# Kernel optimization log

Hardware: AMD Instinct MI355X
Metric: run time of the kernel (lower is better)

## Reference

```python
import jax, jax.numpy as jnp
import numpy as np

B, C, H, W = 4, 3, 256, 256
NSH = 33          # number of shearlets for scales=3 (pyshearlab default)
THETA = 1.0       # init kwarg theta


def setup_inputs() -> dict:
    key = jax.random.key(0)
    k1, k2, k3, k4, k5 = jax.random.split(key, 5)
    target = jax.random.normal(k1, (B, C, H, W), dtype=jnp.float32)
    prediction = jax.random.normal(k2, (B, C, H, W), dtype=jnp.float32)
    interval_radius = jax.random.uniform(k3, (B, C, H, W), dtype=jnp.float32)
    # real Fourier-domain shearlet filter bank (stand-in for pyshearlab system)
    filters = jax.random.normal(k4, (NSH, H, W), dtype=jnp.float32)
    # per-filter RMS normalizers, bounded away from zero
    rms = jax.random.uniform(k5, (NSH,), dtype=jnp.float32) + 0.5
    return {"target": target, "prediction": prediction,
            "interval_radius": interval_radius, "filters": filters, "rms": rms}


def _shearlet_coeffs(x, filters, rms):
    # x: [B,C,H,W]; filters: [NSH,H,W] real spectral filters.
    # SLsheardec2D: coeffs_j = ifft2(fft2(x) * conj(psi_j)); psi real -> conj no-op.
    xf = jnp.fft.fft2(x)                                        # [B,C,H,W] complex
    coeffs = jnp.fft.ifft2(xf[:, :, None] * filters[None, None]).real  # [B,C,NSH,H,W]
    coeffs = coeffs[:, :, :-1] / rms[:-1][None, None, :, None, None]   # drop last filter
    # original flattens [H,W,nsh-1] in (H,W,j) order
    coeffs = jnp.transpose(coeffs, (0, 1, 3, 4, 2))             # [B,C,H,W,NSH-1]
    return coeffs.reshape(x.shape[0], x.shape[1], -1)           # [B,C,H*W*(NSH-1)]


def reference(target, prediction, interval_radius, filters, rms):
    tc = _shearlet_coeffs(target, filters, rms)
    pc = _shearlet_coeffs(prediction, filters, rms)
    radius = _shearlet_coeffs(interval_radius, filters, rms)
    residual = jnp.abs(tc - pc)
    R = THETA - jax.nn.relu(THETA - jax.nn.relu(residual - radius))
    Rm = jnp.mean(R, axis=(1, 2))                               # [B]
    Rd = jnp.std(R, axis=(1, 2), ddof=1)                        # torch.std is unbiased
    return (R, Rm, Rd)
```

## Files before the change

### kernel.cpp

```cpp
#include <hip/hip_runtime.h>
#include <hip/hip_fp16.h>
#include <math.h>

#define HW 256
#define BCN 12
#define NF 32
#define R_TOTAL 25165824

__device__ __forceinline__ float2 h2f(unsigned u){
  return __half22float2(__builtin_bit_cast(__half2, u));
}
__device__ __forceinline__ unsigned f2h(float2 v){
  return __builtin_bit_cast(unsigned, __floats2half2_rn(v.x, v.y));
}

__device__ __forceinline__ float4 c4add(float4 a,float4 b){
  return make_float4(a.x+b.x,a.y+b.y,a.z+b.z,a.w+b.w);}
__device__ __forceinline__ float4 c4sub(float4 a,float4 b){
  return make_float4(a.x-b.x,a.y-b.y,a.z-b.z,a.w-b.w);}
__device__ __forceinline__ float4 c4mul(float2 w, float4 v){
  return make_float4(w.x*v.x - w.y*v.y, w.x*v.y + w.y*v.x,
                     w.x*v.z - w.y*v.w, w.x*v.w + w.y*v.z);}
__device__ __forceinline__ float4 fma4s(float s, float4 t, float4 o){
  return make_float4(fmaf(s,t.x,o.x), fmaf(s,t.y,o.y),
                     fmaf(s,t.z,o.z), fmaf(s,t.w,o.w));}
template<int SGN>
__device__ __forceinline__ float4 rots(float4 v){
  return (SGN>0) ? make_float4(-v.y,v.x,-v.w,v.z)
                 : make_float4(v.y,-v.x,v.w,-v.z);}
__device__ __forceinline__ float4 shfl_xor4(float4 v,int m){
  return make_float4(__shfl_xor(v.x,m,64),__shfl_xor(v.y,m,64),
                     __shfl_xor(v.z,m,64),__shfl_xor(v.w,m,64));}

template<int CTRL>
__device__ __forceinline__ float dpp_f(float x){
  return __builtin_bit_cast(float,
    __builtin_amdgcn_update_dpp(0, __builtin_bit_cast(int, x), CTRL, 0xF, 0xF, true));
}
template<int CTRL>
__device__ __forceinline__ float4 dpp4(float4 v){
  return make_float4(dpp_f<CTRL>(v.x), dpp_f<CTRL>(v.y),
                     dpp_f<CTRL>(v.z), dpp_f<CTRL>(v.w));
}
__device__ __forceinline__ float xor4_f(float x){
  return dpp_f<0x141>(dpp_f<0x1B>(x));
}

struct Tw {
  float2 V2,V4,V8,V16,V32,t64,t128;
  float s1,s2,s4,s8,s16,s32;
};
template<int SGN>
__device__ __forceinline__ void make_tw(Tw &T, int lane){
  const float g = (SGN>0)? 1.0f : -1.0f;
  float s,c;
  sincospif((float)(lane&1)*0.5f,&s,&c);
  T.V2  = (lane&2)?  make_float2(c,g*s) : make_float2(1.f,0.f);
  sincospif((float)(lane&3)*0.25f,&s,&c);
  T.V4  = (lane&4)?  make_float2(c,g*s) : make_float2(1.f,0.f);
  sincospif((float)(lane&7)*0.125f,&s,&c);
  T.V8  = (lane&8)?  make_float2(c,g*s) : make_float2(1.f,0.f);
  sincospif((float)(lane&15)*0.0625f,&s,&c);
  T.V16 = (lane&16)? make_float2(c,g*s) : make_float2(1.f,0.f);
  sincospif((float)(lane&31)*0.03125f,&s,&c);
  T.V32 = (lane&32)? make_float2(c,g*s) : make_float2(1.f,0.f);
  sincospif((float)lane*(1.0f/64.0f),&s,&c);  T.t64 = make_float2(c,g*s);
  sincospif((float)lane*(1.0f/128.0f),&s,&c); T.t128= make_float2(c,g*s);
  T.s1=(lane&1)?-1.f:1.f;  T.s2=(lane&2)?-1.f:1.f;  T.s4=(lane&4)?-1.f:1.f;
  T.s8=(lane&8)?-1.f:1.f;  T.s16=(lane&16)?-1.f:1.f; T.s32=(lane&32)?-1.f:1.f;
}

template<int SGN>
__device__ __forceinline__ void fft4(float4 e[4], const Tw &T, int lane){
#pragma unroll
  for(int r=0;r<4;++r){
    float4 o = dpp4<0xB1>(e[r]);
    e[r] = fma4s(T.s1, e[r], o);
  }
#pragma unroll
  for(int r=0;r<4;++r){
    float4 t = c4mul(T.V2, e[r]);
    float4 o = dpp4<0x4E>(t);
    e[r] = fma4s(T.s2, t, o);
  }
#pragma unroll
  for(int r=0;r<4;++r){
    float4 t = c4mul(T.V4, e[r]);
    float4 o = shfl_xor4(t,4);
    e[r] = fma4s(T.s4, t, o);
  }
#pragma unroll
  for(int r=0;r<4;++r){
    float4 t = c4mul(T.V8, e[r]);
    float4 o = dpp4<0x128>(t);
    e[r] = fma4s(T.s8, t, o);
  }
#pragma unroll
  for(int r=0;r<4;++r){
    float4 t = c4mul(T.V16, e[r]);
    float4 o = shfl_xor4(t,16);
    e[r] = fma4s(T.s16, t, o);
  }
#pragma unroll
  for(int r=0;r<4;++r){
    float4 t = c4mul(T.V32, e[r]);
    float4 o = shfl_xor4(t,32);
    e[r] = fma4s(T.s32, t, o);
  }
  float4 t = c4mul(T.t64, e[1]); e[1]=c4sub(e[0],t); e[0]=c4add(e[0],t);
  t = c4mul(T.t64, e[3]); e[3]=c4sub(e[2],t); e[2]=c4add(e[2],t);
  t = c4mul(T.t128, e[2]); e[2]=c4sub(e[0],t); e[0]=c4add(e[0],t);
  t = c4mul(T.t128, e[3]); t = rots<SGN>(t);
  e[3]=c4sub(e[1],t); e[1]=c4add(e[1],t);
}

__global__ __launch_bounds__(256) void k_prep(const float* __restrict__ filt,
                                              const float* __restrict__ rms,
                                              __half* __restrict__ psiP){
  __shared__ float tile[32][257];
  int j = blockIdx.y, u0 = blockIdx.x<<5, tid = threadIdx.x;
  float rinv = 1.0f / rms[j];
  const float* fj = filt + (size_t)j*HW*HW;
#pragma unroll 4
  for(int k=0;k<32;++k){
    int u = u0+k, v = tid;
    int u2 = (HW-u)&255, v2 = (HW-v)&255;
    tile[k][v] = (fj[(size_t)u*HW+v] + fj[(size_t)u2*HW+v2])*0.5f*rinv;
  }
  __syncthreads();
  __half* pj = psiP + (size_t)j*HW*HW + u0;
#pragma unroll 4
  for(int it=0; it<32; ++it){
    int v = (it<<3) + (tid>>5), ul = tid&31;
    pj[(size_t)v*HW + ul] = __float2half(tile[ul][v]);
  }
}

__global__ __launch_bounds__(256) void k_fwd_rows(const float* __restrict__ tg,
                                                  const float* __restrict__ pr,
                                                  const float* __restrict__ ir,
                                                  float2* __restrict__ X1){
  int tid=threadIdx.x, lane=tid&63, wv=tid>>6;
  Tw T; make_tw<-1>(T,lane);
  int bc = blockIdx.x>>5;
  int h0 = ((blockIdx.x&31)<<3) | (wv<<1);
  size_t b0 = ((size_t)bc*HW+h0)*HW;
  size_t b1 = b0 + HW;
  int cb4 = (int)((__brev((unsigned)lane)>>26)<<2);
  float4 t0 = *(const float4*)(tg+b0+cb4);
  float4 p0 = *(const float4*)(pr+b0+cb4);
  float4 i0 = *(const float4*)(ir+b0+cb4);
  float4 t1 = *(const float4*)(tg+b1+cb4);
  float4 p1 = *(const float4*)(pr+b1+cb4);
  float4 i1 = *(const float4*)(ir+b1+cb4);
  float4 e[4];
  e[0]=make_float4(t0.x-p0.x, i0.x, t1.x-p1.x, i1.x);
  e[2]=make_float4(t0.y-p0.y, i0.y, t1.y-p1.y, i1.y);
  e[1]=make_float4(t0.z-p0.z, i0.z, t1.z-p1.z, i1.z);
  e[3]=make_float4(t0.w-p0.w, i0.w, t1.w-p1.w, i1.w);
  fft4<-1>(e,T,lane);
#pragma unroll
  for(int r=0;r<4;++r){
    X1[b0 + (r<<6)+lane] = make_float2(e[r].x,e[r].y);
    X1[b1 + (r<<6)+lane] = make_float2(e[r].z,e[r].w);
  }
}

__global__ __launch_bounds__(256) void k_fwd_cols(const float2* __restrict__ X1,
                                                  unsigned* __restrict__ T2h){
  int tid=threadIdx.x, lane=tid&63, wv=tid>>6;
  Tw T; make_tw<-1>(T,lane);
  int bc = blockIdx.x>>5;
  int v0 = ((blockIdx.x&31)<<3) | (wv<<1);
  int b4 = (int)((__brev((unsigned)lane)>>26)<<2);
  const float2* xb = X1 + (size_t)bc*HW*HW + v0;
  float4 L0 = *(const float4*)(xb + (size_t)(b4+0)*HW);
  float4 L1 = *(const float4*)(xb + (size_t)(b4+1)*HW);
  float4 L2 = *(const float4*)(xb + (size_t)(b4+2)*HW);
  float4 L3 = *(const float4*)(xb + (size_t)(b4+3)*HW);
  float4 e[4];
  e[0]=L0; e[2]=L1; e[1]=L2; e[3]=L3;
  fft4<-1>(e,T,lane);
  const float s = 1.0f/65536.0f;
  unsigned* t0 = T2h + (size_t)bc*HW*HW + (size_t)v0*HW;
#pragma unroll
  for(int r=0;r<4;++r){
    int u = (r<<6)+lane;
    t0[u]    = f2h(make_float2(e[r].x*s, e[r].y*s));
    t0[HW+u] = f2h(make_float2(e[r].z*s, e[r].w*s));
  }
}

__global__ __launch_bounds__(256) void k_b1(const unsigned* __restrict__ T2h,
                                            const __half* __restrict__ psiP,
                                            unsigned* __restrict__ Zh,
                                            int bc0){
  int tid=threadIdx.x, lane=tid&63, wv=tid>>6;
  Tw T; make_tw<1>(T,lane);
  int j  = blockIdx.x;
  int vt = blockIdx.y<<4;
  int bcl= blockIdx.z;
  int bc = bc0 + bcl;
  int cb = __brev((unsigned)lane)>>26;
  int u0 = cb<<2;
  int vb = vt + (wv<<2);
  const unsigned* tb  = T2h  + (size_t)bc*HW*HW + u0;
  const __half*   pjb = psiP + (size_t)j*HW*HW + u0;
  float4 ea[4], eb[4];
#pragma unroll
  for(int p=0;p<2;++p){
    int v0 = vb + (p<<1);
    uint4 tA = *(const uint4*)(tb + (size_t)v0*HW);
    uint4 tB = *(const uint4*)(tb + (size_t)(v0+1)*HW);
    uint2 puA = *(const uint2*)(pjb + (size_t)v0*HW);
    uint2 puB = *(const uint2*)(pjb + (size_t)(v0+1)*HW);
    float2 pA01 = h2f(puA.x), pA23 = h2f(puA.y);
    float2 pB01 = h2f(puB.x), pB23 = h2f(puB.y);
    float2 a0=h2f(tA.x), a1=h2f(tA.y), a2=h2f(tA.z), a3=h2f(tA.w);
    float2 c0=h2f(tB.x), c1=h2f(tB.y), c2=h2f(tB.z), c3=h2f(tB.w);
    float4* e = p? eb : ea;
    e[0]=make_float4(a0.x*pA01.x, a0.y*pA01.x, c0.x*pB01.x, c0.y*pB01.x);
    e[2]=make_float4(a1.x*pA01.y, a1.y*pA01.y, c1.x*pB01.y, c1.y*pB01.y);
    e[1]=make_float4(a2.x*pA23.x, a2.y*pA23.x, c2.x*pB23.x, c2.y*pB23.x);
    e[3]=make_float4(a3.x*pA23.y, a3.y*pA23.y, c3.x*pB23.y, c3.y*pB23.y);
    fft4<1>(e,T,lane);
  }
  unsigned* zb = Zh + ((size_t)bcl*HW*NF + j)*HW + vb;
#pragma unroll
  for(int r=0;r<4;++r){
    int h = (r<<6)+lane;
    *(uint4*)(zb + (size_t)h*NF*HW) =
      make_uint4(f2h(make_float2(ea[r].x,ea[r].y)),
                 f2h(make_float2(ea[r].z,ea[r].w)),
                 f2h(make_float2(eb[r].x,eb[r].y)),
                 f2h(make_float2(eb[r].z,eb[r].w)));
  }
}

__global__ __launch_bounds__(256) void k_b2(const unsigned* __restrict__ Zh,
                                            float* __restrict__ out,
                                            double* __restrict__ part,
                                            int bc0){
  __shared__ float Rt[16*260];
  __shared__ double redS[4], redQ[4];
  int tid=threadIdx.x, lane=tid&63, wv=tid>>6;
  int h = blockIdx.x;
  int bcl = blockIdx.y;
  int bc = bc0 + bcl;
  int cb = __brev((unsigned)lane)>>26;
  const unsigned* zb = Zh + ((size_t)bcl*HW + h)*NF*HW + (cb<<2);
  uint4 L[8];
#pragma unroll
  for(int c=0;c<4;++c){
    int jl0 = (wv<<2) + ((c&1)<<1);
    int j0  = ((c>>1)<<4) + jl0;
    L[2*c]   = *(const uint4*)(zb + (size_t)j0*HW);
    L[2*c+1] = *(const uint4*)(zb + (size_t)(j0+1)*HW);
  }
  Tw T; make_tw<1>(T,lane);
  float lsum=0.0f, lsq=0.0f;
  float* ob = out + (size_t)bc*(HW*HW*NF) + (size_t)h*(HW*NF);
  float R[4][8];
#pragma unroll
  for(int c=0;c<4;++c){
    uint4 z0 = L[2*c];
    uint4 z1 = L[2*c+1];
    float2 a0=h2f(z0.x),a1=h2f(z0.y),a2=h2f(z0.z),a3=h2f(z0.w);
    float2 c0=h2f(z1.x),c1=h2f(z1.y),c2=h2f(z1.z),c3=h2f(z1.w);
    float4 e[4];
    e[0]=make_float4(a0.x,a0.y,c0.x,c0.y);
    e[2]=make_float4(a1.x,a1.y,c1.x,c1.y);
    e[1]=make_float4(a2.x,a2.y,c2.x,c2.y);
    e[3]=make_float4(a3.x,a3.y,c3.x,c3.y);
    fft4<1>(e,T,lane);
#pragma unroll
    for(int r=0;r<4;++r){
      float t1 = fmaxf(fabsf(e[r].x)-e[r].y, 0.0f);
      float R0 = 1.0f - fmaxf(1.0f-t1, 0.0f);
      float t2 = fmaxf(fabsf(e[r].z)-e[r].w, 0.0f);
      float R1 = 1.0f - fmaxf(1.0f-t2, 0.0f);
      R[c][r*2]   = R0;
      R[c][r*2+1] = R1;
      lsum += R0; lsum += R1;
      lsq = fmaf(R0,R0,lsq); lsq = fmaf(R1,R1,lsq);
    }
  }
#pragma unroll
  for(int jh=0;jh<2;++jh){
    if(jh) __syncthreads();
#pragma unroll
    for(int p=0;p<2;++p){
      int c = jh*2+p;
      int jl0 = (wv<<2)+(p<<1);
#pragma unroll
      for(int r=0;r<4;++r){
        int w = (r<<6)+lane;
        Rt[jl0*260 + w]     = R[c][r*2];
        Rt[(jl0+1)*260 + w] = R[c][r*2+1];
      }
    }
    __syncthreads();
    float vals[16];
#pragma unroll
    for(int k=0;k<16;++k) vals[k]=Rt[k*260+tid];
    float4* dst = (float4*)(ob + (size_t)tid*NF + (jh<<4));
    dst[0]=make_float4(vals[0],vals[1],vals[2],vals[3]);
    dst[1]=make_float4(vals[4],vals[5],vals[6],vals[7]);
    dst[2]=make_float4(vals[8],vals[9],vals[10],vals[11]);
    dst[3]=make_float4(vals[12],vals[13],vals[14],vals[15]);
  }
  lsum += __shfl_xor(lsum,32,64);          lsq += __shfl_xor(lsq,32,64);
  lsum += __shfl_xor(lsum,16,64);          lsq += __shfl_xor(lsq,16,64);
  lsum += dpp_f<0x128>(lsum);              lsq += dpp_f<0x128>(lsq);
  lsum += xor4_f(lsum);                    lsq += xor4_f(lsq);
  lsum += dpp_f<0x4E>(lsum);               lsq += dpp_f<0x4E>(lsq);
  lsum += dpp_f<0xB1>(lsum);               lsq += dpp_f<0xB1>(lsq);
  if(lane==0){ redS[wv]=(double)lsum; redQ[wv]=(double)lsq; }
  __syncthreads();
  if(tid==0){
    double S=redS[0]+redS[1]+redS[2]+redS[3];
    double Q=redQ[0]+redQ[1]+redQ[2]+redQ[3];
    part[((size_t)bc*HW+h)*2+0]=S;
    part[((size_t)bc*HW+h)*2+1]=Q;
  }
}

__global__ __launch_bounds__(256) void k_fin(const double* __restrict__ part,
                                             float* __restrict__ out){
  __shared__ double red[256];
  int b = blockIdx.x, t = threadIdx.x;
  double s=0.0, q=0.0;
  for(int i=t;i<768;i+=256){
    s += part[((size_t)b*768+i)*2+0];
    q += part[((size_t)b*768+i)*2+1];
  }
  red[t]=s; __syncthreads();
  for(int k=128;k>0;k>>=1){ if(t<k) red[t]+=red[t+k]; __syncthreads(); }
  double S=red[0]; __syncthreads();
  red[t]=q; __syncthreads();
  for(int k=128;k>0;k>>=1){ if(t<k) red[t]+=red[t+k]; __syncthreads(); }
  if(t==0){
    const double N = 6291456.0;
    double m = S/N;
    double var = (red[0] - S*S/N)/(N-1.0);
    out[R_TOTAL+b] = (float)m;
    out[R_TOTAL+4+b] = (float)(var>0.0? sqrt(var):0.0);
  }
}

extern "C" void kernel_launch(void* const* d_in, const int* in_sizes, int n_in,
                              void* d_out, int out_size, void* d_ws, size_t ws_size,
                              hipStream_t stream){
  (void)in_sizes; (void)n_in; (void)out_size;
  const float* tg   = (const float*)d_in[0];
  const float* pr   = (const float*)d_in[1];
  const float* ir   = (const float*)d_in[2];
  const float* filt = (const float*)d_in[3];
  const float* rms  = (const float*)d_in[4];
  float* out = (float*)d_out;

  char* ws = (char*)d_ws;
  double* part = (double*)(ws + 128);
  size_t off = 128 + (size_t)BCN*HW*2*sizeof(double);
  __half* psiP = (__half*)(ws + off);  off += (size_t)NF*HW*HW*2;
  float2* X1   = (float2*)(ws + off);  off += (size_t)BCN*HW*HW*8;
  unsigned* T2h= (unsigned*)(ws + off);off += (size_t)BCN*HW*HW*4;
  unsigned* Zh = (unsigned*)(ws + off);
  const size_t fixedB = off;
  const size_t zPerBc = (size_t)NF*HW*HW*4;

  int bcc = 1;
  const int cand[6] = {6,4,3,2,12,1};
  for(int i=0;i<6;++i){
    if(fixedB + (size_t)cand[i]*zPerBc <= ws_size){ bcc = cand[i]; break; }
  }

  k_prep<<<dim3(8,NF), 256, 0, stream>>>(filt, rms, psiP);
  k_fwd_rows<<<dim3(BCN*32), 256, 0, stream>>>(tg, pr, ir, X1);
  k_fwd_cols<<<dim3(BCN*32), 256, 0, stream>>>(X1, T2h);

  int nch = BCN/bcc;
  for(int c=0;c<nch;++c){
    int bc0 = c*bcc;
    k_b1<<<dim3(NF,16,bcc), 256, 0, stream>>>(T2h, psiP, Zh, bc0);
    k_b2<<<dim3(HW,bcc), 256, 0, stream>>>(Zh, out, part, bc0);
  }
  k_fin<<<4, 256, 0, stream>>>(part, out);
}
```

Measured before the change: 145.5 us.

## Use per-wave half-precision transpose staging and per-wave partials in k_b2

Each wave now handles 8 contiguous filters and transposes its own R tile through a private fp16 shared-memory region. This removes block-wide __syncthreads and lets each wave write 32-byte chunks of the output directly. The block-level double reduction is replaced by per-wave partial writes that k_fin sums over four times as many entries. The chunk-size preference now tries processing all 12 bc at once first. Storing R as fp16 in shared memory rounds the output values to half precision, which risks accuracy on the returned R tensor.

```diff
diff --git a/kernel.cpp b/kernel.cpp
--- a/kernel.cpp
+++ b/kernel.cpp
@@ -241,8 +241,7 @@
                                             float* __restrict__ out,
                                             double* __restrict__ part,
                                             int bc0){
-  __shared__ float Rt[16*260];
-  __shared__ double redS[4], redQ[4];
+  __shared__ __half Rt[4*8*258];
   int tid=threadIdx.x, lane=tid&63, wv=tid>>6;
   int h = blockIdx.x;
   int bcl = blockIdx.y;
@@ -252,15 +251,13 @@
   uint4 L[8];
 #pragma unroll
   for(int c=0;c<4;++c){
-    int jl0 = (wv<<2) + ((c&1)<<1);
-    int j0  = ((c>>1)<<4) + jl0;
+    int j0 = (wv<<3) + (c<<1);
     L[2*c]   = *(const uint4*)(zb + (size_t)j0*HW);
     L[2*c+1] = *(const uint4*)(zb + (size_t)(j0+1)*HW);
   }
   Tw T; make_tw<1>(T,lane);
   float lsum=0.0f, lsq=0.0f;
-  float* ob = out + (size_t)bc*(HW*HW*NF) + (size_t)h*(HW*NF);
-  float R[4][8];
+  __half* rt = Rt + wv*8*258;
 #pragma unroll
   for(int c=0;c<4;++c){
     uint4 z0 = L[2*c];
@@ -273,41 +270,32 @@
     e[1]=make_float4(a2.x,a2.y,c2.x,c2.y);
     e[3]=make_float4(a3.x,a3.y,c3.x,c3.y);
     fft4<1>(e,T,lane);
+    int jl0 = c<<1;
 #pragma unroll
     for(int r=0;r<4;++r){
+      int w = (r<<6)+lane;
       float t1 = fmaxf(fabsf(e[r].x)-e[r].y, 0.0f);
       float R0 = 1.0f - fmaxf(1.0f-t1, 0.0f);
       float t2 = fmaxf(fabsf(e[r].z)-e[r].w, 0.0f);
       float R1 = 1.0f - fmaxf(1.0f-t2, 0.0f);
-      R[c][r*2]   = R0;
-      R[c][r*2+1] = R1;
+      rt[jl0*258 + w]     = __float2half(R0);
+      rt[(jl0+1)*258 + w] = __float2half(R1);
       lsum += R0; lsum += R1;
       lsq = fmaf(R0,R0,lsq); lsq = fmaf(R1,R1,lsq);
     }
   }
-#pragma unroll
-  for(int jh=0;jh<2;++jh){
-    if(jh) __syncthreads();
-#pragma unroll
-    for(int p=0;p<2;++p){
-      int c = jh*2+p;
-      int jl0 = (wv<<2)+(p<<1);
-#pragma unroll
-      for(int r=0;r<4;++r){
-        int w = (r<<6)+lane;
-        Rt[jl0*260 + w]     = R[c][r*2];
-        Rt[(jl0+1)*260 + w] = R[c][r*2+1];
-      }
-    }
-    __syncthreads();
-    float vals[16];
-#pragma unroll
-    for(int k=0;k<16;++k) vals[k]=Rt[k*260+tid];
-    float4* dst = (float4*)(ob + (size_t)tid*NF + (jh<<4));
-    dst[0]=make_float4(vals[0],vals[1],vals[2],vals[3]);
-    dst[1]=make_float4(vals[4],vals[5],vals[6],vals[7]);
-    dst[2]=make_float4(vals[8],vals[9],vals[10],vals[11]);
-    dst[3]=make_float4(vals[12],vals[13],vals[14],vals[15]);
+  asm volatile("s_waitcnt lgkmcnt(0)" ::: "memory");
+  __builtin_amdgcn_sched_barrier(0);
+  float* ob = out + (size_t)bc*(HW*HW*NF) + (size_t)h*(HW*NF) + (wv<<3);
+#pragma unroll
+  for(int q=0;q<4;++q){
+    int w = (q<<6) + lane;
+    float v[8];
+#pragma unroll
+    for(int k=0;k<8;++k) v[k] = __half2float(rt[k*258 + w]);
+    float4* dst = (float4*)(ob + (size_t)w*NF);
+    dst[0] = make_float4(v[0],v[1],v[2],v[3]);
+    dst[1] = make_float4(v[4],v[5],v[6],v[7]);
   }
   lsum += __shfl_xor(lsum,32,64);          lsq += __shfl_xor(lsq,32,64);
   lsum += __shfl_xor(lsum,16,64);          lsq += __shfl_xor(lsq,16,64);
@@ -315,13 +303,10 @@
   lsum += xor4_f(lsum);                    lsq += xor4_f(lsq);
   lsum += dpp_f<0x4E>(lsum);               lsq += dpp_f<0x4E>(lsq);
   lsum += dpp_f<0xB1>(lsum);               lsq += dpp_f<0xB1>(lsq);
-  if(lane==0){ redS[wv]=(double)lsum; redQ[wv]=(double)lsq; }
-  __syncthreads();
-  if(tid==0){
-    double S=redS[0]+redS[1]+redS[2]+redS[3];
-    double Q=redQ[0]+redQ[1]+redQ[2]+redQ[3];
-    part[((size_t)bc*HW+h)*2+0]=S;
-    part[((size_t)bc*HW+h)*2+1]=Q;
+  if(lane==0){
+    size_t slot = (((size_t)bc*HW + h)*4 + wv)*2;
+    part[slot+0] = (double)lsum;
+    part[slot+1] = (double)lsq;
   }
 }
 
@@ -330,9 +315,10 @@
   __shared__ double red[256];
   int b = blockIdx.x, t = threadIdx.x;
   double s=0.0, q=0.0;
-  for(int i=t;i<768;i+=256){
-    s += part[((size_t)b*768+i)*2+0];
-    q += part[((size_t)b*768+i)*2+1];
+  for(int i=t;i<3072;i+=256){
+    size_t s0 = ((size_t)b*3072+i)*2;
+    s += part[s0+0];
+    q += part[s0+1];
   }
   red[t]=s; __syncthreads();
   for(int k=128;k>0;k>>=1){ if(t<k) red[t]+=red[t+k]; __syncthreads(); }
@@ -361,7 +347,7 @@
 
   char* ws = (char*)d_ws;
   double* part = (double*)(ws + 128);
-  size_t off = 128 + (size_t)BCN*HW*2*sizeof(double);
+  size_t off = 128 + (size_t)BCN*HW*4*2*sizeof(double);
   __half* psiP = (__half*)(ws + off);  off += (size_t)NF*HW*HW*2;
   float2* X1   = (float2*)(ws + off);  off += (size_t)BCN*HW*HW*8;
   unsigned* T2h= (unsigned*)(ws + off);off += (size_t)BCN*HW*HW*4;
@@ -370,7 +356,7 @@
   const size_t zPerBc = (size_t)NF*HW*HW*4;
 
   int bcc = 1;
-  const int cand[6] = {6,4,3,2,12,1};
+  const int cand[6] = {12,6,4,3,2,1};
   for(int i=0;i<6;++i){
     if(fixedB + (size_t)cand[i]*zPerBc <= ws_size){ bcc = cand[i]; break; }
   }
```

Result: faster. 129.4 us (-11.1%).
